# Kernel tuning notes

Hardware: AMD Instinct MI355X
Metric: run time of the kernel (lower is better)

Reference implementation:

```python
import jax, jax.numpy as jnp
import numpy as np

N_NODES = 50000
N_EDGES = 800000
D_IN = 128
D_OUT = 128


def setup_inputs() -> dict:
    key = jax.random.key(0)
    k1, k2, k3, k4, k5 = jax.random.split(key, 5)
    x = jax.random.normal(k1, (N_NODES, D_IN), dtype=jnp.float32)
    src = jax.random.randint(k2, (N_EDGES,), 0, N_NODES, dtype=jnp.int32)
    dst = jax.random.randint(k3, (N_EDGES,), 0, N_NODES, dtype=jnp.int32)
    # nn.Linear(in_feats, out_feats): weight [out, in], bias [out]
    W = jax.random.normal(k4, (D_OUT, D_IN), dtype=jnp.float32) / np.sqrt(D_IN)
    b = jax.random.normal(k5, (D_OUT,), dtype=jnp.float32) * 0.01
    return {"x": x, "src": src, "dst": dst, "W": W, "b": b}


def reference(x, src, dst, W, b):
    # copy_u('h','m') + sum reduce: h_dst = sum_{e:(u->v)} x[u]
    msgs = x[src]  # [E, D_IN] gather of source features
    h = jax.ops.segment_sum(msgs, dst, num_segments=N_NODES)  # [N, D_IN]
    # linear: h @ W.T + b ; dropout_rate=0.0 -> identity
    out = jnp.einsum('nd,od->no', h, W) + b
    return out
```

## Files before the change

kernel.cpp:

```cpp
#include <hip/hip_runtime.h>

#define N_NODES 50000
#define N_EDGES 800000
#define D 128
#define NB 782
#define NBK 1563
#define SORT_CAP 1024

typedef __attribute__((ext_vector_type(8))) short bf16x8;
typedef __attribute__((ext_vector_type(4))) float floatx4;

__device__ __forceinline__ unsigned short f2bf(float f) {
  unsigned u = __builtin_bit_cast(unsigned, f);
  unsigned r = u + 0x7FFFu + ((u >> 16) & 1u);
  return (unsigned short)(r >> 16);
}
__device__ __forceinline__ float bf2f_lo(unsigned u) {
  return __builtin_bit_cast(float, u << 16);
}
__device__ __forceinline__ float bf2f_hi(unsigned u) {
  return __builtin_bit_cast(float, u & 0xFFFF0000u);
}
__device__ __forceinline__ uint2 pack4bf(float4 v) {
  unsigned a = f2bf(v.x), b = f2bf(v.y), c = f2bf(v.z), d = f2bf(v.w);
  return uint2{a | (b << 16), c | (d << 16)};
}

__global__ __launch_bounds__(256) void wconv_kernel(
    const float* __restrict__ W, unsigned short* __restrict__ wbf) {
  int i = blockIdx.x * 256 + threadIdx.x;
  float4 v = *(const float4*)(W + (size_t)i * 4);
  *(uint2*)(wbf + (size_t)i * 4) = pack4bf(v);
}

#define LDA 136
#define BIN_T 256
#define BIN_CHUNK 4096
#define BIN_BLOCKS 196
#define OFFS_W 1564

struct BinShm {
  unsigned stage[BIN_CHUNK];
  int hcnt[NBK];
  int hstart[NBK];
  int hcur[NBK];
  int wsums[4];
  int tot;
};
struct GemmShm {
  unsigned short As[64 * LDA];
};
union PrepShm {
  BinShm bin;
  GemmShm gemm;
};

__global__ __launch_bounds__(256) void prep_kernel(
    const float* __restrict__ x, const unsigned short* __restrict__ wbf,
    unsigned short* __restrict__ y,
    const int* __restrict__ src, const int* __restrict__ dst,
    unsigned* __restrict__ ebuf, int* __restrict__ offs) {
  __shared__ PrepShm shm;
  int t = threadIdx.x;

  if (blockIdx.x >= BIN_BLOCKS) {
    unsigned short* As = shm.gemm.As;
    int row0 = (blockIdx.x - BIN_BLOCKS) * 64;

    for (int i = t; i < 2048; i += 256) {
      int r = i >> 5;
      int c4 = (i & 31) * 4;
      int gr = row0 + r;
      float4 v = (gr < N_NODES) ? *(const float4*)(x + (size_t)gr * D + c4)
                                : float4{0.f, 0.f, 0.f, 0.f};
      *(uint2*)&As[r * LDA + c4] = pack4bf(v);
    }
    __syncthreads();

    int w = t >> 6;
    int lane = t & 63;
    int ln = lane & 15;
    int quad = lane >> 4;

    floatx4 acc[8];
#pragma unroll
    for (int n = 0; n < 8; ++n) acc[n] = floatx4{0.f, 0.f, 0.f, 0.f};

#pragma unroll
    for (int ks = 0; ks < 4; ++ks) {
      int kc = ks * 32 + quad * 8;
      bf16x8 a = *(const bf16x8*)&As[(w * 16 + ln) * LDA + kc];
#pragma unroll
      for (int n = 0; n < 8; ++n) {
        bf16x8 bf = *(const bf16x8*)&wbf[(size_t)(n * 16 + ln) * D + kc];
        acc[n] = __builtin_amdgcn_mfma_f32_16x16x32_bf16(a, bf, acc[n], 0, 0, 0);
      }
    }

    int gr0 = row0 + w * 16 + quad * 4;
#pragma unroll
    for (int n = 0; n < 8; ++n) {
      int gc = n * 16 + ln;
#pragma unroll
      for (int r = 0; r < 4; ++r) {
        int gr = gr0 + r;
        if (gr < N_NODES) y[(size_t)gr * D + gc] = f2bf(acc[n][r]);
      }
    }
  } else {
    BinShm& B = shm.bin;
    int blk = blockIdx.x;
    int e0 = blk * BIN_CHUNK;
    for (int i = t; i < NBK; i += BIN_T) B.hcnt[i] = 0;
    __syncthreads();

    unsigned pk[16];
    short bk[16];
#pragma unroll
    for (int j = 0; j < 16; ++j) {
      int e = e0 + j * BIN_T + t;
      bk[j] = -1;
      if (e < N_EDGES) {
        int d = dst[e];
        int s = src[e];
        pk[j] = ((unsigned)s << 5) | (unsigned)(d & 31);
        bk[j] = (short)(d >> 5);
        atomicAdd(&B.hcnt[d >> 5], 1);
      }
    }
    __syncthreads();

    int c7[7];
    int s7 = 0;
    int base7 = t * 7;
#pragma unroll
    for (int j = 0; j < 7; ++j) {
      int idx = base7 + j;
      c7[j] = (idx < NBK) ? B.hcnt[idx] : 0;
      s7 += c7[j];
    }
    int incl = s7;
    int lane = t & 63, wid = t >> 6;
#pragma unroll
    for (int off = 1; off < 64; off <<= 1) {
      int n = __shfl_up(incl, off);
      if (lane >= off) incl += n;
    }
    if (lane == 63) B.wsums[wid] = incl;
    __syncthreads();
    int wbase = 0;
    for (int w2 = 0; w2 < wid; ++w2) wbase += B.wsums[w2];
    int run = wbase + incl - s7;
#pragma unroll
    for (int j = 0; j < 7; ++j) {
      int idx = base7 + j;
      if (idx < NBK) { B.hstart[idx] = run; B.hcur[idx] = run; }
      run += c7[j];
    }
    if (t == BIN_T - 1) B.tot = run;
    __syncthreads();

#pragma unroll
    for (int j = 0; j < 16; ++j) {
      if (bk[j] >= 0) {
        int p = atomicAdd(&B.hcur[bk[j]], 1);
        B.stage[p] = pk[j];
      }
    }
    __syncthreads();

    int tot = B.tot;
    unsigned* dseg = ebuf + (size_t)blk * BIN_CHUNK;
    int tot4 = tot >> 2;
    uint4* d4 = (uint4*)dseg;
    const uint4* s4p = (const uint4*)B.stage;
    for (int i = t; i < tot4; i += BIN_T) d4[i] = s4p[i];
    for (int i = (tot & ~3) + t; i < tot; i += BIN_T) dseg[i] = B.stage[i];

    int* orow = offs + (size_t)blk * OFFS_W;
    for (int i = t; i < NBK; i += BIN_T) orow[i] = B.hstart[i];
    if (t == 0) orow[NBK] = tot;
  }
}

__global__ __launch_bounds__(256) void gather_sorted(
    const unsigned short* __restrict__ y, const unsigned* __restrict__ ebuf,
    const int* __restrict__ offs, const float* __restrict__ bias,
    float* __restrict__ out) {
  __shared__ int cnts[32];
  __shared__ int curs[32];
  __shared__ int starts[33];
  __shared__ int sorted[SORT_CAP];
  __shared__ unsigned ec[SORT_CAP];
  __shared__ int wsum2[4];
  __shared__ int segtot;

  int b = blockIdx.x;
  int t = threadIdx.x;
  if (t < 32) cnts[t] = 0;

  int s0 = 0, slen = 0;
  if (t < BIN_BLOCKS) {
    const int* orow = offs + (size_t)t * OFFS_W;
    s0 = orow[b];
    slen = orow[b + 1] - s0;
  }
  int lane = t & 63, wid = t >> 6;
  int v = slen;
#pragma unroll
  for (int off = 1; off < 64; off <<= 1) {
    int n = __shfl_up(v, off);
    if (lane >= off) v += n;
  }
  if (lane == 63) wsum2[wid] = v;
  __syncthreads();
  int wbase = 0;
  for (int w2 = 0; w2 < wid; ++w2) wbase += wsum2[w2];
  int base = wbase + v - slen;
  if (t == 255) segtot = wbase + v;

  const unsigned* myseg = ebuf + (size_t)t * BIN_CHUNK + s0;
  for (int j = 0; j < slen; ++j) {
    int p = base + j;
    if (p < SORT_CAP) ec[p] = myseg[j];
  }
  __syncthreads();

  int cnt = segtot;
  if (cnt > SORT_CAP) cnt = SORT_CAP;

  for (int i = t; i < cnt; i += 256) atomicAdd(&cnts[ec[i] & 31u], 1);
  __syncthreads();

  if (t < 32) {
    int c = cnts[t];
    int vv = c;
#pragma unroll
    for (int off = 1; off < 32; off <<= 1) {
      int n = __shfl_up(vv, off);
      if (t >= off) vv += n;
    }
    starts[t] = vv - c;
    curs[t] = vv - c;
    if (t == 31) starts[32] = vv;
  }
  __syncthreads();

  for (int i = t; i < cnt; i += 256) {
    unsigned u = ec[i];
    int p = atomicAdd(&curs[u & 31u], 1);
    sorted[p] = (int)(u >> 5);
  }
  __syncthreads();

  int wv = t >> 6;
  int g = lane >> 4;
  int l = lane & 15;
  float4 bv0 = *(const float4*)(bias + l * 8);
  float4 bv1 = *(const float4*)(bias + l * 8 + 4);
  for (int n = wv; n < 32; n += 4) {
    int node = b * 32 + n;
    int beg = starts[n];
    int end = starts[n + 1];
    float acc[8] = {0.f, 0.f, 0.f, 0.f, 0.f, 0.f, 0.f, 0.f};
    int i = beg + g;
    for (; i + 12 < end; i += 16) {
      int s0e = sorted[i];
      int s1e = sorted[i + 4];
      int s2e = sorted[i + 8];
      int s3e = sorted[i + 12];
      uint4 u0 = *(const uint4*)(y + (size_t)s0e * D + l * 8);
      uint4 u1 = *(const uint4*)(y + (size_t)s1e * D + l * 8);
      uint4 u2 = *(const uint4*)(y + (size_t)s2e * D + l * 8);
      uint4 u3 = *(const uint4*)(y + (size_t)s3e * D + l * 8);
      acc[0] += (bf2f_lo(u0.x) + bf2f_lo(u1.x)) + (bf2f_lo(u2.x) + bf2f_lo(u3.x));
      acc[1] += (bf2f_hi(u0.x) + bf2f_hi(u1.x)) + (bf2f_hi(u2.x) + bf2f_hi(u3.x));
      acc[2] += (bf2f_lo(u0.y) + bf2f_lo(u1.y)) + (bf2f_lo(u2.y) + bf2f_lo(u3.y));
      acc[3] += (bf2f_hi(u0.y) + bf2f_hi(u1.y)) + (bf2f_hi(u2.y) + bf2f_hi(u3.y));
      acc[4] += (bf2f_lo(u0.z) + bf2f_lo(u1.z)) + (bf2f_lo(u2.z) + bf2f_lo(u3.z));
      acc[5] += (bf2f_hi(u0.z) + bf2f_hi(u1.z)) + (bf2f_hi(u2.z) + bf2f_hi(u3.z));
      acc[6] += (bf2f_lo(u0.w) + bf2f_lo(u1.w)) + (bf2f_lo(u2.w) + bf2f_lo(u3.w));
      acc[7] += (bf2f_hi(u0.w) + bf2f_hi(u1.w)) + (bf2f_hi(u2.w) + bf2f_hi(u3.w));
    }
    for (; i < end; i += 4) {
      int s = sorted[i];
      uint4 u = *(const uint4*)(y + (size_t)s * D + l * 8);
      acc[0] += bf2f_lo(u.x); acc[1] += bf2f_hi(u.x);
      acc[2] += bf2f_lo(u.y); acc[3] += bf2f_hi(u.y);
      acc[4] += bf2f_lo(u.z); acc[5] += bf2f_hi(u.z);
      acc[6] += bf2f_lo(u.w); acc[7] += bf2f_hi(u.w);
    }
#pragma unroll
    for (int j = 0; j < 8; ++j) {
      acc[j] += __shfl_xor(acc[j], 16);
      acc[j] += __shfl_xor(acc[j], 32);
    }
    if (g == 0 && node < N_NODES) {
      float4 r0 = {acc[0] + bv0.x, acc[1] + bv0.y, acc[2] + bv0.z, acc[3] + bv0.w};
      float4 r1 = {acc[4] + bv1.x, acc[5] + bv1.y, acc[6] + bv1.z, acc[7] + bv1.w};
      float* op = out + (size_t)node * D + l * 8;
      *(float4*)op = r0;
      *(float4*)(op + 4) = r1;
    }
  }
}

__global__ __launch_bounds__(256) void hist_kernel(
    const int* __restrict__ dst, int* __restrict__ counts) {
  int e = blockIdx.x * 256 + threadIdx.x;
  if (e < N_EDGES) atomicAdd(&counts[dst[e]], 1);
}

#define SBLK 196
__global__ __launch_bounds__(256) void reduce_kernel(
    const int* __restrict__ counts, int* __restrict__ blockSums) {
  int i = blockIdx.x * 256 + threadIdx.x;
  int v = (i < N_NODES) ? counts[i] : 0;
#pragma unroll
  for (int off = 32; off; off >>= 1) v += __shfl_down(v, off);
  __shared__ int ws[4];
  int lane = threadIdx.x & 63, wid = threadIdx.x >> 6;
  if (lane == 0) ws[wid] = v;
  __syncthreads();
  if (threadIdx.x == 0) blockSums[blockIdx.x] = ws[0] + ws[1] + ws[2] + ws[3];
}

__global__ __launch_bounds__(256) void scan_kernel2(
    const int* __restrict__ counts, const int* __restrict__ blockSums,
    int* __restrict__ offsets, int* __restrict__ cursor) {
  int b = blockIdx.x;
  int t = threadIdx.x;
  int lane = t & 63, wid = t >> 6;
  int pv = (t < b) ? blockSums[t] : 0;
#pragma unroll
  for (int off = 32; off; off >>= 1) pv += __shfl_down(pv, off);
  __shared__ int ws[4];
  __shared__ int wsum[4];
  __shared__ int base_s;
  if (lane == 0) ws[wid] = pv;
  __syncthreads();
  if (t == 0) base_s = ws[0] + ws[1] + ws[2] + ws[3];
  int i = b * 256 + t;
  int c = (i < N_NODES) ? counts[i] : 0;
  int v = c;
#pragma unroll
  for (int off = 1; off < 64; off <<= 1) {
    int n = __shfl_up(v, off);
    if (lane >= off) v += n;
  }
  if (lane == 63) wsum[wid] = v;
  __syncthreads();
  int wbase = 0;
  for (int w2 = 0; w2 < wid; ++w2) wbase += wsum[w2];
  int excl = base_s + wbase + v - c;
  if (i < N_NODES) {
    offsets[i] = excl;
    cursor[i] = excl;
    if (i == N_NODES - 1) offsets[N_NODES] = excl + c;
  }
}

__global__ __launch_bounds__(256) void fill_kernel(
    const int* __restrict__ src, const int* __restrict__ dst,
    int* __restrict__ cursor, int* __restrict__ esrc) {
  int e = blockIdx.x * 256 + threadIdx.x;
  if (e >= N_EDGES) return;
  int pos = atomicAdd(&cursor[dst[e]], 1);
  esrc[pos] = src[e];
}

__global__ __launch_bounds__(256) void gemm_xw(
    const float* __restrict__ x, const float* __restrict__ W,
    unsigned short* __restrict__ y) {
  __shared__ unsigned short As[64 * LDA];
  __shared__ unsigned short Ws[128 * LDA];
  int t = threadIdx.x;
  int row0 = blockIdx.x * 64;
  for (int i = t; i < 2048; i += 256) {
    int r = i >> 5;
    int c4 = (i & 31) * 4;
    int gr = row0 + r;
    float4 v = (gr < N_NODES) ? *(const float4*)(x + (size_t)gr * D + c4)
                              : float4{0.f, 0.f, 0.f, 0.f};
    *(uint2*)&As[r * LDA + c4] = pack4bf(v);
  }
  for (int i = t; i < 4096; i += 256) {
    int r = i >> 5;
    int c4 = (i & 31) * 4;
    float4 wv = *(const float4*)(W + (size_t)r * D + c4);
    *(uint2*)&Ws[r * LDA + c4] = pack4bf(wv);
  }
  __syncthreads();
  int w = t >> 6;
  int lane = t & 63;
  int ln = lane & 15;
  int quad = lane >> 4;
  floatx4 acc[8];
#pragma unroll
  for (int n = 0; n < 8; ++n) acc[n] = floatx4{0.f, 0.f, 0.f, 0.f};
#pragma unroll
  for (int ks = 0; ks < 4; ++ks) {
    int kc = ks * 32 + quad * 8;
    bf16x8 a = *(const bf16x8*)&As[(w * 16 + ln) * LDA + kc];
#pragma unroll
    for (int n = 0; n < 8; ++n) {
      bf16x8 bf = *(const bf16x8*)&Ws[(n * 16 + ln) * LDA + kc];
      acc[n] = __builtin_amdgcn_mfma_f32_16x16x32_bf16(a, bf, acc[n], 0, 0, 0);
    }
  }
  int gr0 = row0 + w * 16 + quad * 4;
#pragma unroll
  for (int n = 0; n < 8; ++n) {
    int gc = n * 16 + ln;
#pragma unroll
    for (int r = 0; r < 4; ++r) {
      int gr = gr0 + r;
      if (gr < N_NODES) y[(size_t)gr * D + gc] = f2bf(acc[n][r]);
    }
  }
}

__global__ __launch_bounds__(256) void gather_ybf_kernel(
    const unsigned short* __restrict__ y, const int* __restrict__ esrc,
    const int* __restrict__ offsets, const float* __restrict__ bias,
    float* __restrict__ out) {
  int node = blockIdx.x * 4 + (threadIdx.x >> 6);
  if (node >= N_NODES) return;
  int lane = threadIdx.x & 63;
  int g = lane >> 4;
  int l = lane & 15;
  int beg = offsets[node];
  int end = offsets[node + 1];
  float acc[8] = {0.f, 0.f, 0.f, 0.f, 0.f, 0.f, 0.f, 0.f};
  int i = beg + g;
  for (; i + 4 < end; i += 8) {
    int s0 = esrc[i];
    int s1 = esrc[i + 4];
    uint4 u0 = *(const uint4*)(y + (size_t)s0 * D + l * 8);
    uint4 u1 = *(const uint4*)(y + (size_t)s1 * D + l * 8);
    acc[0] += bf2f_lo(u0.x) + bf2f_lo(u1.x);
    acc[1] += bf2f_hi(u0.x) + bf2f_hi(u1.x);
    acc[2] += bf2f_lo(u0.y) + bf2f_lo(u1.y);
    acc[3] += bf2f_hi(u0.y) + bf2f_hi(u1.y);
    acc[4] += bf2f_lo(u0.z) + bf2f_lo(u1.z);
    acc[5] += bf2f_hi(u0.z) + bf2f_hi(u1.z);
    acc[6] += bf2f_lo(u0.w) + bf2f_lo(u1.w);
    acc[7] += bf2f_hi(u0.w) + bf2f_hi(u1.w);
  }
  if (i < end) {
    int s = esrc[i];
    uint4 u = *(const uint4*)(y + (size_t)s * D + l * 8);
    acc[0] += bf2f_lo(u.x); acc[1] += bf2f_hi(u.x);
    acc[2] += bf2f_lo(u.y); acc[3] += bf2f_hi(u.y);
    acc[4] += bf2f_lo(u.z); acc[5] += bf2f_hi(u.z);
    acc[6] += bf2f_lo(u.w); acc[7] += bf2f_hi(u.w);
  }
#pragma unroll
  for (int j = 0; j < 8; ++j) {
    acc[j] += __shfl_xor(acc[j], 16);
    acc[j] += __shfl_xor(acc[j], 32);
  }
  if (g == 0) {
    const float* bp = bias + l * 8;
    float4 r0 = {acc[0] + bp[0], acc[1] + bp[1], acc[2] + bp[2], acc[3] + bp[3]};
    float4 r1 = {acc[4] + bp[4], acc[5] + bp[5], acc[6] + bp[6], acc[7] + bp[7]};
    float* op = out + (size_t)node * D + l * 8;
    *(float4*)op = r0;
    *(float4*)(op + 4) = r1;
  }
}

__global__ __launch_bounds__(256) void scatter_kernel(
    const float* __restrict__ x, const int* __restrict__ src,
    const int* __restrict__ dst, float* __restrict__ out) {
  int gtid = blockIdx.x * 256 + threadIdx.x;
  int e = gtid >> 6;
  int lane = threadIdx.x & 63;
  if (e >= N_EDGES) return;
  float2 v = ((const float2*)(x + (size_t)src[e] * D))[lane];
  float* orow = out + (size_t)dst[e] * D + lane * 2;
  atomicAdd(orow + 0, v.x);
  atomicAdd(orow + 1, v.y);
}

__global__ __launch_bounds__(256) void transform_kernel(
    float* __restrict__ out, const float* __restrict__ W,
    const float* __restrict__ bias) {
  constexpr int RPB = 64;
  constexpr int HP = 132;
  __shared__ float Hs[RPB][HP];
  int t = threadIdx.x;
  int row0 = blockIdx.x * RPB;
  int nr = min(RPB, N_NODES - row0);
  {
    const float4* g = (const float4*)(out + (size_t)row0 * D);
    for (int i = t; i < nr * (D / 4); i += 256) {
      int r = i >> 5;
      int c = (i & 31) * 4;
      *(float4*)&Hs[r][c] = g[i];
    }
  }
  __syncthreads();
  int tx = t & 15;
  int ty = t >> 4;
  int r0 = ty * 4;
  for (int half = 0; half < 2; ++half) {
    int oc0 = half * 64 + tx * 4;
    const float* Wb = W + (size_t)oc0 * D;
    float4 a0 = {0.f, 0.f, 0.f, 0.f}, a1 = {0.f, 0.f, 0.f, 0.f};
    float4 a2 = {0.f, 0.f, 0.f, 0.f}, a3 = {0.f, 0.f, 0.f, 0.f};
#pragma unroll 8
    for (int k = 0; k < D; k += 4) {
      float4 w0 = *(const float4*)(Wb + 0 * D + k);
      float4 w1 = *(const float4*)(Wb + 1 * D + k);
      float4 w2 = *(const float4*)(Wb + 2 * D + k);
      float4 w3 = *(const float4*)(Wb + 3 * D + k);
      float4 h0 = *(const float4*)&Hs[r0 + 0][k];
      float4 h1 = *(const float4*)&Hs[r0 + 1][k];
      float4 h2 = *(const float4*)&Hs[r0 + 2][k];
      float4 h3 = *(const float4*)&Hs[r0 + 3][k];
#define DOT(hv, wv) fmaf((hv).w, (wv).w, fmaf((hv).z, (wv).z, fmaf((hv).y, (wv).y, (hv).x * (wv).x)))
      a0.x += DOT(h0, w0); a0.y += DOT(h0, w1); a0.z += DOT(h0, w2); a0.w += DOT(h0, w3);
      a1.x += DOT(h1, w0); a1.y += DOT(h1, w1); a1.z += DOT(h1, w2); a1.w += DOT(h1, w3);
      a2.x += DOT(h2, w0); a2.y += DOT(h2, w1); a2.z += DOT(h2, w2); a2.w += DOT(h2, w3);
      a3.x += DOT(h3, w0); a3.y += DOT(h3, w1); a3.z += DOT(h3, w2); a3.w += DOT(h3, w3);
#undef DOT
    }
    float4 bv = *(const float4*)(bias + oc0);
    a0.x += bv.x; a0.y += bv.y; a0.z += bv.z; a0.w += bv.w;
    a1.x += bv.x; a1.y += bv.y; a1.z += bv.z; a1.w += bv.w;
    a2.x += bv.x; a2.y += bv.y; a2.z += bv.z; a2.w += bv.w;
    a3.x += bv.x; a3.y += bv.y; a3.z += bv.z; a3.w += bv.w;
    if (r0 + 0 < nr) *(float4*)(out + (size_t)(row0 + r0 + 0) * D + oc0) = a0;
    if (r0 + 1 < nr) *(float4*)(out + (size_t)(row0 + r0 + 1) * D + oc0) = a1;
    if (r0 + 2 < nr) *(float4*)(out + (size_t)(row0 + r0 + 2) * D + oc0) = a2;
    if (r0 + 3 < nr) *(float4*)(out + (size_t)(row0 + r0 + 3) * D + oc0) = a3;
  }
}

extern "C" void kernel_launch(void* const* d_in, const int* in_sizes, int n_in,
                              void* d_out, int out_size, void* d_ws, size_t ws_size,
                              hipStream_t stream) {
  const float* x = (const float*)d_in[0];
  const int* src = (const int*)d_in[1];
  const int* dst = (const int*)d_in[2];
  const float* W = (const float*)d_in[3];
  const float* b = (const float*)d_in[4];
  float* out = (float*)d_out;

  const size_t ybytes = (size_t)N_NODES * D * sizeof(unsigned short);
  const size_t ebytes = (size_t)BIN_BLOCKS * BIN_CHUNK * sizeof(unsigned);
  const size_t obytes = (size_t)BIN_BLOCKS * OFFS_W * sizeof(int);
  const size_t wbytes = (size_t)D * D * sizeof(unsigned short);

  if (ws_size >= ybytes + ebytes + obytes + wbytes) {
    unsigned short* y = (unsigned short*)d_ws;
    unsigned* ebuf = (unsigned*)((char*)d_ws + ybytes);
    int* offs = (int*)((char*)ebuf + ebytes);
    unsigned short* wbf = (unsigned short*)((char*)offs + obytes);

    wconv_kernel<<<16, 256, 0, stream>>>(W, wbf);
    prep_kernel<<<BIN_BLOCKS + NB, 256, 0, stream>>>(x, wbf, y, src, dst, ebuf, offs);
    gather_sorted<<<NBK, 256, 0, stream>>>(y, ebuf, offs, b, out);
    return;
  }

  const size_t A = 50048;
  const size_t head_ints = 3 * A + 256 + (size_t)N_EDGES;
  const size_t need_csr = head_ints * sizeof(int) + ybytes;

  if (ws_size >= need_csr) {
    int* counts     = (int*)d_ws;
    int* offsets    = counts + A;
    int* cursor     = offsets + A;
    int* blockSums  = cursor + A;
    int* esrc       = blockSums + 256;
    unsigned short* y = (unsigned short*)(esrc + N_EDGES);

    hipMemsetAsync(counts, 0, N_NODES * sizeof(int), stream);
    hist_kernel<<<(N_EDGES + 255) / 256, 256, 0, stream>>>(dst, counts);
    reduce_kernel<<<SBLK, 256, 0, stream>>>(counts, blockSums);
    scan_kernel2<<<SBLK, 256, 0, stream>>>(counts, blockSums, offsets, cursor);
    fill_kernel<<<(N_EDGES + 255) / 256, 256, 0, stream>>>(src, dst, cursor, esrc);
    gemm_xw<<<NB, 256, 0, stream>>>(x, W, y);
    gather_ybf_kernel<<<(N_NODES + 3) / 4, 256, 0, stream>>>(y, esrc, offsets, b, out);
  } else {
    hipMemsetAsync(out, 0, (size_t)N_NODES * D * sizeof(float), stream);
    scatter_kernel<<<N_EDGES / 4, 256, 0, stream>>>(x, src, dst, out);
    transform_kernel<<<(N_NODES + 63) / 64, 256, 0, stream>>>(out, W, b);
  }
}
```

Before: 138.0 us.

## Halve destination bucket width to 16 nodes and merge histogram arrays

Destination buckets shrink from 32 to 16 nodes, which doubles the bucket count to 3125 so that twice as many gather blocks each handle fewer nodes. The binning kernel now uses one shared array for counts, starts and cursors, writing offsets before the scatter, which lowers LDS use. The goal is more parallelism and occupancy in the gather phase, at the cost of a larger offsets table that each gather block must read. Launch grid sizes elsewhere have to match the new bucket count, and SORT_CAP drops to 512, so overflow could become a concern.

```diff
diff --git a/kernel.cpp b/kernel.cpp
--- a/kernel.cpp
+++ b/kernel.cpp
@@ -4,8 +4,8 @@
 #define N_EDGES 800000
 #define D 128
 #define NB 782
-#define NBK 1563
-#define SORT_CAP 1024
+#define NBK 3125
+#define SORT_CAP 512
 
 typedef __attribute__((ext_vector_type(8))) short bf16x8;
 typedef __attribute__((ext_vector_type(4))) float floatx4;
@@ -37,13 +37,11 @@
 #define BIN_T 256
 #define BIN_CHUNK 4096
 #define BIN_BLOCKS 196
-#define OFFS_W 1564
+#define OFFS_W 3126
 
 struct BinShm {
   unsigned stage[BIN_CHUNK];
-  int hcnt[NBK];
-  int hstart[NBK];
-  int hcur[NBK];
+  int hstart[NBK + 1];
   int wsums[4];
   int tot;
 };
@@ -111,7 +109,7 @@
     BinShm& B = shm.bin;
     int blk = blockIdx.x;
     int e0 = blk * BIN_CHUNK;
-    for (int i = t; i < NBK; i += BIN_T) B.hcnt[i] = 0;
+    for (int i = t; i < NBK; i += BIN_T) B.hstart[i] = 0;
     __syncthreads();
 
     unsigned pk[16];
@@ -123,23 +121,23 @@
       if (e < N_EDGES) {
         int d = dst[e];
         int s = src[e];
-        pk[j] = ((unsigned)s << 5) | (unsigned)(d & 31);
-        bk[j] = (short)(d >> 5);
-        atomicAdd(&B.hcnt[d >> 5], 1);
+        pk[j] = ((unsigned)s << 4) | (unsigned)(d & 15);
+        bk[j] = (short)(d >> 4);
+        atomicAdd(&B.hstart[d >> 4], 1);
       }
     }
     __syncthreads();
 
-    int c7[7];
-    int s7 = 0;
-    int base7 = t * 7;
-#pragma unroll
-    for (int j = 0; j < 7; ++j) {
-      int idx = base7 + j;
-      c7[j] = (idx < NBK) ? B.hcnt[idx] : 0;
-      s7 += c7[j];
-    }
-    int incl = s7;
+    int c13[13];
+    int s13 = 0;
+    int base13 = t * 13;
+#pragma unroll
+    for (int j = 0; j < 13; ++j) {
+      int idx = base13 + j;
+      c13[j] = (idx < NBK) ? B.hstart[idx] : 0;
+      s13 += c13[j];
+    }
+    int incl = s13;
     int lane = t & 63, wid = t >> 6;
 #pragma unroll
     for (int off = 1; off < 64; off <<= 1) {
@@ -150,20 +148,24 @@
     __syncthreads();
     int wbase = 0;
     for (int w2 = 0; w2 < wid; ++w2) wbase += B.wsums[w2];
-    int run = wbase + incl - s7;
-#pragma unroll
-    for (int j = 0; j < 7; ++j) {
-      int idx = base7 + j;
-      if (idx < NBK) { B.hstart[idx] = run; B.hcur[idx] = run; }
-      run += c7[j];
-    }
-    if (t == BIN_T - 1) B.tot = run;
+    int run = wbase + incl - s13;
+#pragma unroll
+    for (int j = 0; j < 13; ++j) {
+      int idx = base13 + j;
+      if (idx < NBK) B.hstart[idx] = run;
+      run += c13[j];
+    }
+    if (t == BIN_T - 1) { B.hstart[NBK] = run; B.tot = run; }
+    __syncthreads();
+
+    int* orow = offs + (size_t)blk * OFFS_W;
+    for (int i = t; i <= NBK; i += BIN_T) orow[i] = B.hstart[i];
     __syncthreads();
 
 #pragma unroll
     for (int j = 0; j < 16; ++j) {
       if (bk[j] >= 0) {
-        int p = atomicAdd(&B.hcur[bk[j]], 1);
+        int p = atomicAdd(&B.hstart[bk[j]], 1);
         B.stage[p] = pk[j];
       }
     }
@@ -176,10 +178,6 @@
     const uint4* s4p = (const uint4*)B.stage;
     for (int i = t; i < tot4; i += BIN_T) d4[i] = s4p[i];
     for (int i = (tot & ~3) + t; i < tot; i += BIN_T) dseg[i] = B.stage[i];
-
-    int* orow = offs + (size_t)blk * OFFS_W;
-    for (int i = t; i < NBK; i += BIN_T) orow[i] = B.hstart[i];
-    if (t == 0) orow[NBK] = tot;
   }
 }
 
@@ -187,9 +185,9 @@
     const unsigned short* __restrict__ y, const unsigned* __restrict__ ebuf,
     const int* __restrict__ offs, const float* __restrict__ bias,
     float* __restrict__ out) {
-  __shared__ int cnts[32];
-  __shared__ int curs[32];
-  __shared__ int starts[33];
+  __shared__ int cnts[16];
+  __shared__ int curs[16];
+  __shared__ int starts[17];
   __shared__ int sorted[SORT_CAP];
   __shared__ unsigned ec[SORT_CAP];
   __shared__ int wsum2[4];
@@ -197,7 +195,7 @@
 
   int b = blockIdx.x;
   int t = threadIdx.x;
-  if (t < 32) cnts[t] = 0;
+  if (t < 16) cnts[t] = 0;
 
   int s0 = 0, slen = 0;
   if (t < BIN_BLOCKS) {
@@ -229,27 +227,27 @@
   int cnt = segtot;
   if (cnt > SORT_CAP) cnt = SORT_CAP;
 
-  for (int i = t; i < cnt; i += 256) atomicAdd(&cnts[ec[i] & 31u], 1);
-  __syncthreads();
-
-  if (t < 32) {
+  for (int i = t; i < cnt; i += 256) atomicAdd(&cnts[ec[i] & 15u], 1);
+  __syncthreads();
+
+  if (t < 16) {
     int c = cnts[t];
     int vv = c;
 #pragma unroll
-    for (int off = 1; off < 32; off <<= 1) {
+    for (int off = 1; off < 16; off <<= 1) {
       int n = __shfl_up(vv, off);
       if (t >= off) vv += n;
     }
     starts[t] = vv - c;
     curs[t] = vv - c;
-    if (t == 31) starts[32] = vv;
+    if (t == 15) starts[16] = vv;
   }
   __syncthreads();
 
   for (int i = t; i < cnt; i += 256) {
     unsigned u = ec[i];
-    int p = atomicAdd(&curs[u & 31u], 1);
-    sorted[p] = (int)(u >> 5);
+    int p = atomicAdd(&curs[u & 15u], 1);
+    sorted[p] = (int)(u >> 4);
   }
   __syncthreads();
 
@@ -258,8 +256,8 @@
   int l = lane & 15;
   float4 bv0 = *(const float4*)(bias + l * 8);
   float4 bv1 = *(const float4*)(bias + l * 8 + 4);
-  for (int n = wv; n < 32; n += 4) {
-    int node = b * 32 + n;
+  for (int n = wv; n < 16; n += 4) {
+    int node = b * 16 + n;
     int beg = starts[n];
     int end = starts[n + 1];
     float acc[8] = {0.f, 0.f, 0.f, 0.f, 0.f, 0.f, 0.f, 0.f};
```

After: 140.1 us. Within noise of the previous version (+1.5%).
